# Kernel tuning notes

Measured on AMD Instinct MI355X. Metric: run time of the kernel, lower is better.

## Reference

```python
import jax, jax.numpy as jnp
import numpy as np

N_NODES = 100000
N_EDGES = 1600000
H, D, DE = 4, 32, 32  # heads, node_out_feats, edge_out_feats
NEG_SLOPE = 0.2


def setup_inputs() -> dict:
    key = jax.random.key(0)
    ks = jax.random.split(key, 10)
    return {
        "node_inputs": jax.random.normal(ks[0], (N_NODES, 128), jnp.float32),
        "edge_inputs": jax.random.normal(ks[1], (N_EDGES, 16), jnp.float32),
        "src": jax.random.randint(ks[2], (N_EDGES,), 0, N_NODES, jnp.int32),
        "dst": jax.random.randint(ks[3], (N_EDGES,), 0, N_NODES, jnp.int32),
        "W_fc": jax.random.normal(ks[4], (128, H * D), jnp.float32) * 0.1,
        "attn_src_p": jax.random.normal(ks[5], (1, H, D), jnp.float32) * 0.1,
        "attn_dst_p": jax.random.normal(ks[6], (1, H, D), jnp.float32) * 0.1,
        "W_edge": jax.random.normal(ks[7], (16, H * DE), jnp.float32) * 0.1,
        "attn_edge_p": jax.random.normal(ks[8], (1, H, DE), jnp.float32) * 0.1,
        "W_res": jax.random.normal(ks[9], (128, H * D), jnp.float32) * 0.1,
        "bias_p": jnp.zeros((H * D,), jnp.float32),
    }


def reference(node_inputs, edge_inputs, src, dst, W_fc, attn_src_p,
              attn_dst_p, W_edge, attn_edge_p, W_res, bias_p):
    N = node_inputs.shape[0]
    # node projection: [N, H, D]
    feat = (node_inputs @ W_fc).reshape(N, H, D)
    # per-node attention logits [N, H]
    a_src = (feat * attn_src_p).sum(-1)
    a_dst = (feat * attn_dst_p).sum(-1)
    # edge-feature attention logits [E, H]
    feat_e = (edge_inputs @ W_edge).reshape(-1, H, DE)
    a_edge = (feat_e * attn_edge_p).sum(-1)
    # per-edge score: u_add_v + edge term, then LeakyReLU
    e = a_src[src] + a_dst[dst] + a_edge                 # [E, H]
    e = jnp.where(e > 0, e, NEG_SLOPE * e)
    # edge softmax grouped by destination node
    emax = jax.lax.stop_gradient(jax.ops.segment_max(e, dst, num_segments=N))
    ex = jnp.exp(e - emax[dst])
    denom = jax.ops.segment_sum(ex, dst, num_segments=N)
    attn = ex / denom[dst]                               # [E, H]
    # weighted scatter-aggregate of source features
    msg = feat[src] * attn[:, :, None]                   # [E, H, D]
    x = jax.ops.segment_sum(msg, dst, num_segments=N)    # [N, H, D]
    # residual + bias
    x = x + (node_inputs @ W_res).reshape(N, H, D)
    x = x + bias_p.reshape(H, D)
    return x
```

## Files before the change

### kernel.cpp

```cpp
#include <hip/hip_runtime.h>
#include <math.h>

#define NNODES_FEAT 128
#define HD 128
#define H 4
#define D 32
#define EDGE_F 16
#define NEG_SLOPE 0.2f

typedef _Float16 f16;
typedef _Float16 f16x2 __attribute__((ext_vector_type(2)));
typedef _Float16 f16x4 __attribute__((ext_vector_type(4)));
typedef _Float16 f16x8 __attribute__((ext_vector_type(8)));
typedef float f32x4 __attribute__((ext_vector_type(4)));

union ExPack { float2 f; f16x4 h; };

__global__ void k_wedge(const float* __restrict__ W_edge,
                        const float* __restrict__ attn_edge,
                        float* __restrict__ w_eh) {
    int t = threadIdx.x;
    int k = t >> 2;
    int h = t & 3;
    float s = 0.f;
    for (int d = 0; d < D; ++d)
        s += W_edge[k * HD + h * D + d] * attn_edge[h * D + d];
    w_eh[k * H + h] = s;
}

__global__ __launch_bounds__(256) void k_wt(const float* __restrict__ Wfc,
                                            const float* __restrict__ Wres,
                                            f16* __restrict__ Wt) {
    int i = blockIdx.x * 256 + threadIdx.x;
    int n = i >> 7, k = i & 127;
    float v = (n < 128) ? Wfc[k * HD + n] : Wres[k * HD + (n - 128)];
    Wt[(size_t)n * 128 + k] = (f16)v;
}

#define LDK 136
__global__ __launch_bounds__(256) void k_gemm_mfma(
    const float* __restrict__ A, const f16* __restrict__ Wt,
    const float* __restrict__ bias, f16* __restrict__ feat16,
    float* __restrict__ out, int N) {
    __shared__ f16 As[64 * LDK];
    __shared__ f16 Bs[128 * LDK];
    int tid = threadIdx.x;
    int wave = tid >> 6, lane = tid & 63;
    int m0 = blockIdx.x * 64;

    for (int c = tid; c < 64 * 32; c += 256) {
        int r = c >> 5, cc = (c & 31) * 4;
        int gr = m0 + r;
        float4 v = make_float4(0.f, 0.f, 0.f, 0.f);
        if (gr < N) v = *(const float4*)(A + (size_t)gr * 128 + cc);
        f16x4 h = {(f16)v.x, (f16)v.y, (f16)v.z, (f16)v.w};
        *(f16x4*)(&As[r * LDK + cc]) = h;
    }

    int am = lane & 15, aq = lane >> 4;
    int arow = wave * 16 + am;
    int orow0 = m0 + wave * 16 + aq * 4;

    for (int cb = 0; cb < 2; ++cb) {
        if (cb) __syncthreads();
        const f16* Wblk = Wt + (size_t)cb * 128 * 128;
        for (int c = tid; c < 128 * 16; c += 256) {
            int r = c >> 4, cc = (c & 15) * 8;
            float4 v = *(const float4*)(Wblk + (size_t)r * 128 + cc);
            *(float4*)(&Bs[r * LDK + cc]) = v;
        }
        __syncthreads();

        f32x4 acc[8];
#pragma unroll
        for (int nt = 0; nt < 8; ++nt) acc[nt] = (f32x4){0.f, 0.f, 0.f, 0.f};
#pragma unroll
        for (int kc = 0; kc < 4; ++kc) {
            f16x8 a = *(const f16x8*)(&As[arow * LDK + kc * 32 + aq * 8]);
#pragma unroll
            for (int nt = 0; nt < 8; ++nt) {
                f16x8 b = *(const f16x8*)(&Bs[(nt * 16 + am) * LDK + kc * 32 + aq * 8]);
                acc[nt] = __builtin_amdgcn_mfma_f32_16x16x32_f16(a, b, acc[nt], 0, 0, 0);
            }
        }

        if (cb == 0) {
#pragma unroll
            for (int nt = 0; nt < 8; ++nt) {
                int col = nt * 16 + am;
#pragma unroll
                for (int r = 0; r < 4; ++r) {
                    int row = orow0 + r;
                    if (row < N) feat16[(size_t)row * 128 + col] = (f16)acc[nt][r];
                }
            }
        } else {
#pragma unroll
            for (int nt = 0; nt < 8; ++nt) {
                int col = nt * 16 + am;
                float bv = bias[col];
#pragma unroll
                for (int r = 0; r < 4; ++r) {
                    int row = orow0 + r;
                    if (row < N) out[(size_t)row * 128 + col] = acc[nt][r] + bv;
                }
            }
        }
    }
}

__global__ __launch_bounds__(256) void k_attn_nodes(
    const f16* __restrict__ feat16, const float* __restrict__ attn_src,
    const float* __restrict__ attn_dst, float* __restrict__ a_src,
    float* __restrict__ a_dst, int N) {
    int g = blockIdx.x * 256 + threadIdx.x;
    int n = g >> 2, h = g & 3;
    if (n >= N) return;
    const f16* f = feat16 + (size_t)n * HD + h * D;
    const float* w1 = attn_src + h * D;
    const float* w2 = attn_dst + h * D;
    float s1 = 0.f, s2 = 0.f;
#pragma unroll
    for (int d = 0; d < D; d += 2) {
        f16x2 fv = *(const f16x2*)(f + d);
        float f0 = (float)fv.x, f1 = (float)fv.y;
        s1 += f0 * w1[d] + f1 * w1[d + 1];
        s2 += f0 * w2[d] + f1 * w2[d + 1];
    }
    a_src[n * H + h] = s1;
    a_dst[n * H + h] = s2;
}

__global__ __launch_bounds__(256) void k_count_mlp(
    const float* __restrict__ edge_inputs, const int* __restrict__ dst,
    const float* __restrict__ w_eh, int* __restrict__ deg,
    int* __restrict__ rank, float2* __restrict__ ae16, int E) {
    __shared__ float weh_s[EDGE_F * H];
    if (threadIdx.x < EDGE_F * H) weh_s[threadIdx.x] = w_eh[threadIdx.x];
    __syncthreads();

    int base = blockIdx.x * 512 + threadIdx.x;
    int e0 = base, e1 = base + 256;
    bool v0 = e0 < E, v1 = e1 < E;

    int d0 = v0 ? dst[e0] : 0;
    int d1 = v1 ? dst[e1] : 0;

    float4 xa[4], xb[4];
    if (v0) {
        const float* x = edge_inputs + (size_t)e0 * EDGE_F;
        xa[0] = *(const float4*)(x);      xa[1] = *(const float4*)(x + 4);
        xa[2] = *(const float4*)(x + 8);  xa[3] = *(const float4*)(x + 12);
    }
    if (v1) {
        const float* x = edge_inputs + (size_t)e1 * EDGE_F;
        xb[0] = *(const float4*)(x);      xb[1] = *(const float4*)(x + 4);
        xb[2] = *(const float4*)(x + 8);  xb[3] = *(const float4*)(x + 12);
    }

    int r0 = v0 ? atomicAdd(deg + d0, 1) : 0;
    int r1 = v1 ? atomicAdd(deg + d1, 1) : 0;

    if (v0) {
        float ae0 = 0.f, ae1 = 0.f, ae2 = 0.f, ae3 = 0.f;
        const float* xs = (const float*)xa;
#pragma unroll
        for (int k = 0; k < EDGE_F; ++k) {
            float xv = xs[k];
            ae0 += xv * weh_s[k * H + 0];
            ae1 += xv * weh_s[k * H + 1];
            ae2 += xv * weh_s[k * H + 2];
            ae3 += xv * weh_s[k * H + 3];
        }
        ExPack p;
        p.h = (f16x4){(f16)ae0, (f16)ae1, (f16)ae2, (f16)ae3};
        ae16[e0] = p.f;
        rank[e0] = r0;
    }
    if (v1) {
        float ae0 = 0.f, ae1 = 0.f, ae2 = 0.f, ae3 = 0.f;
        const float* xs = (const float*)xb;
#pragma unroll
        for (int k = 0; k < EDGE_F; ++k) {
            float xv = xs[k];
            ae0 += xv * weh_s[k * H + 0];
            ae1 += xv * weh_s[k * H + 1];
            ae2 += xv * weh_s[k * H + 2];
            ae3 += xv * weh_s[k * H + 3];
        }
        ExPack p;
        p.h = (f16x4){(f16)ae0, (f16)ae1, (f16)ae2, (f16)ae3};
        ae16[e1] = p.f;
        rank[e1] = r1;
    }
}

__global__ __launch_bounds__(256) void k_scan_partial(
    const int* __restrict__ deg, int* __restrict__ partial, int N) {
    __shared__ int sdata[256];
    int t = threadIdx.x;
    int base = blockIdx.x * 1024 + t * 4;
    int s = 0;
#pragma unroll
    for (int j = 0; j < 4; ++j) { int i = base + j; if (i < N) s += deg[i]; }
    sdata[t] = s;
    __syncthreads();
    for (int off = 128; off > 0; off >>= 1) {
        if (t < off) sdata[t] += sdata[t + off];
        __syncthreads();
    }
    if (t == 0) partial[blockIdx.x] = sdata[0];
}

__global__ __launch_bounds__(256) void k_scan_top(
    int* __restrict__ partial, int* __restrict__ offs, int nb, int N) {
    __shared__ int sdata[256];
    int t = threadIdx.x;
    int v = (t < nb) ? partial[t] : 0;
    sdata[t] = v;
    __syncthreads();
    for (int off = 1; off < 256; off <<= 1) {
        int add = (t >= off) ? sdata[t - off] : 0;
        __syncthreads();
        sdata[t] += add;
        __syncthreads();
    }
    int excl = (t == 0) ? 0 : sdata[t - 1];
    if (t < nb) partial[t] = excl;
    if (t == nb - 1) offs[N] = sdata[t];
}

__global__ __launch_bounds__(256) void k_scan_final(
    int* __restrict__ deg_offs, const int* __restrict__ partial, int N) {
    __shared__ int sdata[256];
    int t = threadIdx.x;
    int base = blockIdx.x * 1024 + t * 4;
    int v[4]; int s = 0;
#pragma unroll
    for (int j = 0; j < 4; ++j) { int i = base + j; v[j] = (i < N) ? deg_offs[i] : 0; s += v[j]; }
    sdata[t] = s;
    __syncthreads();
    for (int off = 1; off < 256; off <<= 1) {
        int add = (t >= off) ? sdata[t - off] : 0;
        __syncthreads();
        sdata[t] += add;
        __syncthreads();
    }
    int excl = partial[blockIdx.x] + ((t == 0) ? 0 : sdata[t - 1]);
#pragma unroll
    for (int j = 0; j < 4; ++j) {
        int i = base + j;
        if (i < N) { deg_offs[i] = excl; excl += v[j]; }
    }
}

__global__ __launch_bounds__(256) void k_edge_fill(
    const int* __restrict__ src, const int* __restrict__ dst,
    const int* __restrict__ rank, const float2* __restrict__ ae16,
    const float* __restrict__ a_src, const float* __restrict__ a_dst,
    const int* __restrict__ offs, float4* __restrict__ rec, int E) {
    int base = blockIdx.x * 512 + threadIdx.x;
    int e0 = base, e1 = base + 256;
    bool v0 = e0 < E, v1 = e1 < E;

    int s0 = v0 ? src[e0] : 0, s1 = v1 ? src[e1] : 0;
    int d0 = v0 ? dst[e0] : 0, d1 = v1 ? dst[e1] : 0;
    int r0 = v0 ? rank[e0] : 0, r1 = v1 ? rank[e1] : 0;
    float2 q0 = v0 ? ae16[e0] : make_float2(0.f, 0.f);
    float2 q1 = v1 ? ae16[e1] : make_float2(0.f, 0.f);

    float4 as0 = *(const float4*)(a_src + s0 * H);
    float4 as1 = *(const float4*)(a_src + s1 * H);
    float4 ad0 = *(const float4*)(a_dst + d0 * H);
    float4 ad1 = *(const float4*)(a_dst + d1 * H);
    int p0 = offs[d0] + r0;
    int p1 = offs[d1] + r1;

    if (v0) {
        ExPack qa; qa.f = q0;
        float ev[H];
        ev[0] = as0.x + ad0.x + (float)qa.h[0];
        ev[1] = as0.y + ad0.y + (float)qa.h[1];
        ev[2] = as0.z + ad0.z + (float)qa.h[2];
        ev[3] = as0.w + ad0.w + (float)qa.h[3];
#pragma unroll
        for (int h = 0; h < H; ++h) {
            float t = ev[h];
            t = t > 0.f ? t : NEG_SLOPE * t;
            ev[h] = __expf(t);
        }
        ExPack p;
        p.h = (f16x4){(f16)ev[0], (f16)ev[1], (f16)ev[2], (f16)ev[3]};
        float4 r;
        r.x = __int_as_float(s0);
        r.y = p.f.x;
        r.z = p.f.y;
        r.w = 0.f;
        rec[p0] = r;
    }
    if (v1) {
        ExPack qa; qa.f = q1;
        float ev[H];
        ev[0] = as1.x + ad1.x + (float)qa.h[0];
        ev[1] = as1.y + ad1.y + (float)qa.h[1];
        ev[2] = as1.z + ad1.z + (float)qa.h[2];
        ev[3] = as1.w + ad1.w + (float)qa.h[3];
#pragma unroll
        for (int h = 0; h < H; ++h) {
            float t = ev[h];
            t = t > 0.f ? t : NEG_SLOPE * t;
            ev[h] = __expf(t);
        }
        ExPack p;
        p.h = (f16x4){(f16)ev[0], (f16)ev[1], (f16)ev[2], (f16)ev[3]};
        float4 r;
        r.x = __int_as_float(s1);
        r.y = p.f.x;
        r.z = p.f.y;
        r.w = 0.f;
        rec[p1] = r;
    }
}

__device__ __forceinline__ float exsel(float a, float b, int hword, int hshift) {
    unsigned u = __float_as_uint(hword ? b : a);
    unsigned short us = (unsigned short)(u >> hshift);
    f16 hv;
    __builtin_memcpy(&hv, &us, 2);
    return (float)hv;
}

__global__ __launch_bounds__(256) void k_aggr(
    const f16* __restrict__ feat16, const float4* __restrict__ rec,
    const int* __restrict__ offs, float* __restrict__ out, int N) {
    int wave = threadIdx.x >> 6;
    int lane = threadIdx.x & 63;
    int n = blockIdx.x * 4 + wave;
    if (n >= N) return;
    int beg = offs[n], end = offs[n + 1];
    if (end <= beg) return;
    int hword = (lane >> 5) & 1;
    int hshift = ((lane >> 4) & 1) * 16;
    size_t c0 = (size_t)2 * lane;
    float num0 = 0.f, num1 = 0.f, den = 0.f;
    int i = beg;
    for (; i + 3 < end; i += 4) {
        float4 r0 = rec[i], r1 = rec[i + 1], r2 = rec[i + 2], r3 = rec[i + 3];
        int s0 = __float_as_int(r0.x), s1 = __float_as_int(r1.x);
        int s2 = __float_as_int(r2.x), s3 = __float_as_int(r3.x);
        f16x2 f0 = *(const f16x2*)(feat16 + (size_t)s0 * HD + c0);
        f16x2 f1 = *(const f16x2*)(feat16 + (size_t)s1 * HD + c0);
        f16x2 f2 = *(const f16x2*)(feat16 + (size_t)s2 * HD + c0);
        f16x2 f3 = *(const f16x2*)(feat16 + (size_t)s3 * HD + c0);
        float e0 = exsel(r0.y, r0.z, hword, hshift);
        float e1 = exsel(r1.y, r1.z, hword, hshift);
        float e2 = exsel(r2.y, r2.z, hword, hshift);
        float e3 = exsel(r3.y, r3.z, hword, hshift);
        num0 += e0 * (float)f0.x + e1 * (float)f1.x + e2 * (float)f2.x + e3 * (float)f3.x;
        num1 += e0 * (float)f0.y + e1 * (float)f1.y + e2 * (float)f2.y + e3 * (float)f3.y;
        den += e0 + e1 + e2 + e3;
    }
    for (; i < end; ++i) {
        float4 r0 = rec[i];
        int s0 = __float_as_int(r0.x);
        f16x2 f0 = *(const f16x2*)(feat16 + (size_t)s0 * HD + c0);
        float e0 = exsel(r0.y, r0.z, hword, hshift);
        num0 += e0 * (float)f0.x;
        num1 += e0 * (float)f0.y;
        den += e0;
    }
    float inv = 1.f / den;
    size_t o = (size_t)n * HD + c0;
    float2 v = *(float2*)(out + o);
    v.x += num0 * inv;
    v.y += num1 * inv;
    *(float2*)(out + o) = v;
}

extern "C" void kernel_launch(void* const* d_in, const int* in_sizes, int n_in,
                              void* d_out, int out_size, void* d_ws, size_t ws_size,
                              hipStream_t stream) {
    const float* node_inputs = (const float*)d_in[0];
    const float* edge_inputs = (const float*)d_in[1];
    const int*   src         = (const int*)d_in[2];
    const int*   dst         = (const int*)d_in[3];
    const float* W_fc        = (const float*)d_in[4];
    const float* attn_src_p  = (const float*)d_in[5];
    const float* attn_dst_p  = (const float*)d_in[6];
    const float* W_edge      = (const float*)d_in[7];
    const float* attn_edge_p = (const float*)d_in[8];
    const float* W_res       = (const float*)d_in[9];
    const float* bias_p      = (const float*)d_in[10];

    int N = in_sizes[0] / NNODES_FEAT;
    int E = in_sizes[2];

    float* out = (float*)d_out;

    f16*    feat16  = (f16*)d_ws;
    float4* rec     = (float4*)(feat16 + (size_t)N * HD);
    f16*    Wt      = (f16*)(rec + (size_t)E);
    float*  a_src   = (float*)(Wt + 256 * 128);
    float*  a_dst   = a_src + (size_t)N * H;
    float*  w_eh    = a_dst + (size_t)N * H;
    int*    deg     = (int*)(w_eh + 64);
    int*    offs    = deg;
    int*    partial = deg + (N + 2);
    int*    rank    = partial + 128;
    float2* ae16    = (float2*)(rank + (size_t)E);

    hipMemsetAsync(deg, 0, (size_t)(N + 2) * sizeof(int), stream);

    k_wedge<<<1, 64, 0, stream>>>(W_edge, attn_edge_p, w_eh);
    k_wt<<<(256 * 128) / 256, 256, 0, stream>>>(W_fc, W_res, Wt);

    int gb = (N + 63) / 64;
    k_gemm_mfma<<<gb, 256, 0, stream>>>(node_inputs, Wt, bias_p, feat16, out, N);

    int nb = (N * H + 255) / 256;
    k_attn_nodes<<<nb, 256, 0, stream>>>(feat16, attn_src_p, attn_dst_p, a_src, a_dst, N);

    int eb = (E + 511) / 512;
    k_count_mlp<<<eb, 256, 0, stream>>>(edge_inputs, dst, w_eh, deg, rank, ae16, E);
    int sb = (N + 1023) / 1024;
    k_scan_partial<<<sb, 256, 0, stream>>>(deg, partial, N);
    k_scan_top<<<1, 256, 0, stream>>>(partial, offs, sb, N);
    k_scan_final<<<sb, 256, 0, stream>>>(deg, partial, N);

    k_edge_fill<<<eb, 256, 0, stream>>>(src, dst, rank, ae16, a_src, a_dst,
                                        offs, rec, E);

    int ab = (N + 3) / 4;
    k_aggr<<<ab, 256, 0, stream>>>(feat16, rec, offs, out, N);
}
```

Before: 455.5 us.

## Fuse edge logit and exp into count kernel, split-wave aggregation with wider loads

Moves the per-edge logit, LeakyReLU and exp computation into the degree-counting kernel, so the permute kernel only scatters precomputed values into CSR order with nontemporal stores and 4 edges per thread. The aggregation kernel now splits each wave into two halves that process alternate edges, using 4-wide f16 feature loads and a cross-half shuffle reduction, which halves the serial loop length per node. The attention-node kernel uses 8-wide f16 loads. The trade-off is extra gathers of a_src/a_dst in the atomic-heavy count kernel and more shuffle work per node.

```diff
diff --git a/kernel.cpp b/kernel.cpp
--- a/kernel.cpp
+++ b/kernel.cpp
@@ -121,20 +121,25 @@
     const float* w2 = attn_dst + h * D;
     float s1 = 0.f, s2 = 0.f;
 #pragma unroll
-    for (int d = 0; d < D; d += 2) {
-        f16x2 fv = *(const f16x2*)(f + d);
-        float f0 = (float)fv.x, f1 = (float)fv.y;
-        s1 += f0 * w1[d] + f1 * w1[d + 1];
-        s2 += f0 * w2[d] + f1 * w2[d + 1];
+    for (int dd = 0; dd < D; dd += 8) {
+        f16x8 fv = *(const f16x8*)(f + dd);
+#pragma unroll
+        for (int j = 0; j < 8; ++j) {
+            float fx = (float)fv[j];
+            s1 += fx * w1[dd + j];
+            s2 += fx * w2[dd + j];
+        }
     }
     a_src[n * H + h] = s1;
     a_dst[n * H + h] = s2;
 }
 
-__global__ __launch_bounds__(256) void k_count_mlp(
-    const float* __restrict__ edge_inputs, const int* __restrict__ dst,
-    const float* __restrict__ w_eh, int* __restrict__ deg,
-    int* __restrict__ rank, float2* __restrict__ ae16, int E) {
+__global__ __launch_bounds__(256) void k_edge_logit(
+    const float* __restrict__ edge_inputs, const int* __restrict__ src,
+    const int* __restrict__ dst, const float* __restrict__ w_eh,
+    const float* __restrict__ a_src, const float* __restrict__ a_dst,
+    int* __restrict__ deg, int* __restrict__ rank,
+    float2* __restrict__ evp, int E) {
     __shared__ float weh_s[EDGE_F * H];
     if (threadIdx.x < EDGE_F * H) weh_s[threadIdx.x] = w_eh[threadIdx.x];
     __syncthreads();
@@ -143,8 +148,8 @@
     int e0 = base, e1 = base + 256;
     bool v0 = e0 < E, v1 = e1 < E;
 
-    int d0 = v0 ? dst[e0] : 0;
-    int d1 = v1 ? dst[e1] : 0;
+    int s0 = v0 ? src[e0] : 0, s1 = v1 ? src[e1] : 0;
+    int d0 = v0 ? dst[e0] : 0, d1 = v1 ? dst[e1] : 0;
 
     float4 xa[4], xb[4];
     if (v0) {
@@ -157,6 +162,11 @@
         xb[0] = *(const float4*)(x);      xb[1] = *(const float4*)(x + 4);
         xb[2] = *(const float4*)(x + 8);  xb[3] = *(const float4*)(x + 12);
     }
+
+    float4 as0 = *(const float4*)(a_src + s0 * H);
+    float4 ad0 = *(const float4*)(a_dst + d0 * H);
+    float4 as1 = *(const float4*)(a_src + s1 * H);
+    float4 ad1 = *(const float4*)(a_dst + d1 * H);
 
     int r0 = v0 ? atomicAdd(deg + d0, 1) : 0;
     int r1 = v1 ? atomicAdd(deg + d1, 1) : 0;
@@ -172,9 +182,20 @@
             ae2 += xv * weh_s[k * H + 2];
             ae3 += xv * weh_s[k * H + 3];
         }
+        float ev[H];
+        ev[0] = as0.x + ad0.x + ae0;
+        ev[1] = as0.y + ad0.y + ae1;
+        ev[2] = as0.z + ad0.z + ae2;
+        ev[3] = as0.w + ad0.w + ae3;
+#pragma unroll
+        for (int h = 0; h < H; ++h) {
+            float t = ev[h];
+            t = t > 0.f ? t : NEG_SLOPE * t;
+            ev[h] = __expf(t);
+        }
         ExPack p;
-        p.h = (f16x4){(f16)ae0, (f16)ae1, (f16)ae2, (f16)ae3};
-        ae16[e0] = p.f;
+        p.h = (f16x4){(f16)ev[0], (f16)ev[1], (f16)ev[2], (f16)ev[3]};
+        evp[e0] = p.f;
         rank[e0] = r0;
     }
     if (v1) {
@@ -188,9 +209,20 @@
             ae2 += xv * weh_s[k * H + 2];
             ae3 += xv * weh_s[k * H + 3];
         }
+        float ev[H];
+        ev[0] = as1.x + ad1.x + ae0;
+        ev[1] = as1.y + ad1.y + ae1;
+        ev[2] = as1.z + ad1.z + ae2;
+        ev[3] = as1.w + ad1.w + ae3;
+#pragma unroll
+        for (int h = 0; h < H; ++h) {
+            float t = ev[h];
+            t = t > 0.f ? t : NEG_SLOPE * t;
+            ev[h] = __expf(t);
+        }
         ExPack p;
-        p.h = (f16x4){(f16)ae0, (f16)ae1, (f16)ae2, (f16)ae3};
-        ae16[e1] = p.f;
+        p.h = (f16x4){(f16)ev[0], (f16)ev[1], (f16)ev[2], (f16)ev[3]};
+        evp[e1] = p.f;
         rank[e1] = r1;
     }
 }
@@ -254,71 +286,33 @@
     }
 }
 
-__global__ __launch_bounds__(256) void k_edge_fill(
+__global__ __launch_bounds__(256) void k_permute(
     const int* __restrict__ src, const int* __restrict__ dst,
-    const int* __restrict__ rank, const float2* __restrict__ ae16,
-    const float* __restrict__ a_src, const float* __restrict__ a_dst,
-    const int* __restrict__ offs, float4* __restrict__ rec, int E) {
-    int base = blockIdx.x * 512 + threadIdx.x;
-    int e0 = base, e1 = base + 256;
-    bool v0 = e0 < E, v1 = e1 < E;
-
-    int s0 = v0 ? src[e0] : 0, s1 = v1 ? src[e1] : 0;
-    int d0 = v0 ? dst[e0] : 0, d1 = v1 ? dst[e1] : 0;
-    int r0 = v0 ? rank[e0] : 0, r1 = v1 ? rank[e1] : 0;
-    float2 q0 = v0 ? ae16[e0] : make_float2(0.f, 0.f);
-    float2 q1 = v1 ? ae16[e1] : make_float2(0.f, 0.f);
-
-    float4 as0 = *(const float4*)(a_src + s0 * H);
-    float4 as1 = *(const float4*)(a_src + s1 * H);
-    float4 ad0 = *(const float4*)(a_dst + d0 * H);
-    float4 ad1 = *(const float4*)(a_dst + d1 * H);
-    int p0 = offs[d0] + r0;
-    int p1 = offs[d1] + r1;
-
-    if (v0) {
-        ExPack qa; qa.f = q0;
-        float ev[H];
-        ev[0] = as0.x + ad0.x + (float)qa.h[0];
-        ev[1] = as0.y + ad0.y + (float)qa.h[1];
-        ev[2] = as0.z + ad0.z + (float)qa.h[2];
-        ev[3] = as0.w + ad0.w + (float)qa.h[3];
-#pragma unroll
-        for (int h = 0; h < H; ++h) {
-            float t = ev[h];
-            t = t > 0.f ? t : NEG_SLOPE * t;
-            ev[h] = __expf(t);
-        }
-        ExPack p;
-        p.h = (f16x4){(f16)ev[0], (f16)ev[1], (f16)ev[2], (f16)ev[3]};
-        float4 r;
-        r.x = __int_as_float(s0);
-        r.y = p.f.x;
-        r.z = p.f.y;
-        r.w = 0.f;
-        rec[p0] = r;
-    }
-    if (v1) {
-        ExPack qa; qa.f = q1;
-        float ev[H];
-        ev[0] = as1.x + ad1.x + (float)qa.h[0];
-        ev[1] = as1.y + ad1.y + (float)qa.h[1];
-        ev[2] = as1.z + ad1.z + (float)qa.h[2];
-        ev[3] = as1.w + ad1.w + (float)qa.h[3];
-#pragma unroll
-        for (int h = 0; h < H; ++h) {
-            float t = ev[h];
-            t = t > 0.f ? t : NEG_SLOPE * t;
-            ev[h] = __expf(t);
-        }
-        ExPack p;
-        p.h = (f16x4){(f16)ev[0], (f16)ev[1], (f16)ev[2], (f16)ev[3]};
-        float4 r;
-        r.x = __int_as_float(s1);
-        r.y = p.f.x;
-        r.z = p.f.y;
-        r.w = 0.f;
-        rec[p1] = r;
+    const int* __restrict__ rank, const float2* __restrict__ evp,
+    const int* __restrict__ offs, f32x4* __restrict__ rec, int E) {
+    int base = blockIdx.x * 1024 + threadIdx.x;
+    int s[4], d[4], r[4]; float2 q[4]; bool v[4];
+#pragma unroll
+    for (int j = 0; j < 4; ++j) {
+        int e = base + j * 256;
+        v[j] = e < E;
+        s[j] = v[j] ? src[e] : 0;
+        d[j] = v[j] ? dst[e] : 0;
+        r[j] = v[j] ? rank[e] : 0;
+        q[j] = v[j] ? evp[e] : make_float2(0.f, 0.f);
+    }
+    int pos[4];
+#pragma unroll
+    for (int j = 0; j < 4; ++j) pos[j] = offs[d[j]] + r[j];
+#pragma unroll
+    for (int j = 0; j < 4; ++j) {
+        if (!v[j]) continue;
+        f32x4 rr;
+        rr[0] = __int_as_float(s[j]);
+        rr[1] = q[j].x;
+        rr[2] = q[j].y;
+        rr[3] = 0.f;
+        __builtin_nontemporal_store(rr, &rec[pos[j]]);
     }
 }
 
@@ -331,7 +325,7 @@
 }
 
 __global__ __launch_bounds__(256) void k_aggr(
-    const f16* __restrict__ feat16, const float4* __restrict__ rec,
+    const f16* __restrict__ feat16, const f32x4* __restrict__ rec,
     const int* __restrict__ offs, float* __restrict__ out, int N) {
     int wave = threadIdx.x >> 6;
     int lane = threadIdx.x & 63;
@@ -339,42 +333,64 @@
     if (n >= N) return;
     int beg = offs[n], end = offs[n + 1];
     if (end <= beg) return;
-    int hword = (lane >> 5) & 1;
-    int hshift = ((lane >> 4) & 1) * 16;
-    size_t c0 = (size_t)2 * lane;
-    float num0 = 0.f, num1 = 0.f, den = 0.f;
+    int half = lane >> 5;
+    int l = lane & 31;
+    int hword = (l >> 4) & 1;
+    int hshift = ((l >> 3) & 1) * 16;
+    size_t c0 = (size_t)l * 4;
+    float num0 = 0.f, num1 = 0.f, num2 = 0.f, num3 = 0.f, den = 0.f;
     int i = beg;
     for (; i + 3 < end; i += 4) {
-        float4 r0 = rec[i], r1 = rec[i + 1], r2 = rec[i + 2], r3 = rec[i + 3];
-        int s0 = __float_as_int(r0.x), s1 = __float_as_int(r1.x);
-        int s2 = __float_as_int(r2.x), s3 = __float_as_int(r3.x);
-        f16x2 f0 = *(const f16x2*)(feat16 + (size_t)s0 * HD + c0);
-        f16x2 f1 = *(const f16x2*)(feat16 + (size_t)s1 * HD + c0);
-        f16x2 f2 = *(const f16x2*)(feat16 + (size_t)s2 * HD + c0);
-        f16x2 f3 = *(const f16x2*)(feat16 + (size_t)s3 * HD + c0);
-        float e0 = exsel(r0.y, r0.z, hword, hshift);
-        float e1 = exsel(r1.y, r1.z, hword, hshift);
-        float e2 = exsel(r2.y, r2.z, hword, hshift);
-        float e3 = exsel(r3.y, r3.z, hword, hshift);
-        num0 += e0 * (float)f0.x + e1 * (float)f1.x + e2 * (float)f2.x + e3 * (float)f3.x;
-        num1 += e0 * (float)f0.y + e1 * (float)f1.y + e2 * (float)f2.y + e3 * (float)f3.y;
-        den += e0 + e1 + e2 + e3;
-    }
-    for (; i < end; ++i) {
-        float4 r0 = rec[i];
-        int s0 = __float_as_int(r0.x);
-        f16x2 f0 = *(const f16x2*)(feat16 + (size_t)s0 * HD + c0);
-        float e0 = exsel(r0.y, r0.z, hword, hshift);
-        num0 += e0 * (float)f0.x;
-        num1 += e0 * (float)f0.y;
-        den += e0;
-    }
-    float inv = 1.f / den;
-    size_t o = (size_t)n * HD + c0;
-    float2 v = *(float2*)(out + o);
-    v.x += num0 * inv;
-    v.y += num1 * inv;
-    *(float2*)(out + o) = v;
+        f32x4 ra = __builtin_nontemporal_load(&rec[i + half]);
+        f32x4 rb = __builtin_nontemporal_load(&rec[i + 2 + half]);
+        int sa = __float_as_int(ra[0]), sb = __float_as_int(rb[0]);
+        f16x4 fa = *(const f16x4*)(feat16 + (size_t)sa * HD + c0);
+        f16x4 fb = *(const f16x4*)(feat16 + (size_t)sb * HD + c0);
+        float ea = exsel(ra[1], ra[2], hword, hshift);
+        float eb = exsel(rb[1], rb[2], hword, hshift);
+        num0 += ea * (float)fa[0] + eb * (float)fb[0];
+        num1 += ea * (float)fa[1] + eb * (float)fb[1];
+        num2 += ea * (float)fa[2] + eb * (float)fb[2];
+        num3 += ea * (float)fa[3] + eb * (float)fb[3];
+        den  += ea + eb;
+    }
+    for (; i + 1 < end; i += 2) {
+        f32x4 ra = __builtin_nontemporal_load(&rec[i + half]);
+        int sa = __float_as_int(ra[0]);
+        f16x4 fa = *(const f16x4*)(feat16 + (size_t)sa * HD + c0);
+        float ea = exsel(ra[1], ra[2], hword, hshift);
+        num0 += ea * (float)fa[0];
+        num1 += ea * (float)fa[1];
+        num2 += ea * (float)fa[2];
+        num3 += ea * (float)fa[3];
+        den += ea;
+    }
+    if (i < end) {
+        f32x4 ra = __builtin_nontemporal_load(&rec[i]);
+        int sa = __float_as_int(ra[0]);
+        f16x4 fa = *(const f16x4*)(feat16 + (size_t)sa * HD + c0);
+        float ea = half ? 0.f : exsel(ra[1], ra[2], hword, hshift);
+        num0 += ea * (float)fa[0];
+        num1 += ea * (float)fa[1];
+        num2 += ea * (float)fa[2];
+        num3 += ea * (float)fa[3];
+        den += ea;
+    }
+    num0 += __shfl_xor(num0, 32);
+    num1 += __shfl_xor(num1, 32);
+    num2 += __shfl_xor(num2, 32);
+    num3 += __shfl_xor(num3, 32);
+    den  += __shfl_xor(den, 32);
+    if (half == 0) {
+        float inv = 1.f / den;
+        float* o = out + (size_t)n * HD + c0;
+        float4 v = *(float4*)o;
+        v.x += num0 * inv;
+        v.y += num1 * inv;
+        v.z += num2 * inv;
+        v.w += num3 * inv;
+        *(float4*)o = v;
+    }
 }
 
 extern "C" void kernel_launch(void* const* d_in, const int* in_sizes, int n_in,
@@ -398,7 +414,7 @@
     float* out = (float*)d_out;
 
     f16*    feat16  = (f16*)d_ws;
-    float4* rec     = (float4*)(feat16 + (size_t)N * HD);
+    f32x4*  rec     = (f32x4*)(feat16 + (size_t)N * HD);
     f16*    Wt      = (f16*)(rec + (size_t)E);
     float*  a_src   = (float*)(Wt + 256 * 128);
     float*  a_dst   = a_src + (size_t)N * H;
@@ -407,7 +423,7 @@
     int*    offs    = deg;
     int*    partial = deg + (N + 2);
     int*    rank    = partial + 128;
-    float2* ae16    = (float2*)(rank + (size_t)E);
+    float2* evp     = (float2*)(rank + (size_t)E);
 
     hipMemsetAsync(deg, 0, (size_t)(N + 2) * sizeof(int), stream);
 
@@ -421,14 +437,16 @@
     k_attn_nodes<<<nb, 256, 0, stream>>>(feat16, attn_src_p, attn_dst_p, a_src, a_dst, N);
 
     int eb = (E + 511) / 512;
-    k_count_mlp<<<eb, 256, 0, stream>>>(edge_inputs, dst, w_eh, deg, rank, ae16, E);
+    k_edge_logit<<<eb, 256, 0, stream>>>(edge_inputs, src, dst, w_eh, a_src, a_dst,
+                                         deg, rank, evp, E);
+
     int sb = (N + 1023) / 1024;
     k_scan_partial<<<sb, 256, 0, stream>>>(deg, partial, N);
     k_scan_top<<<1, 256, 0, stream>>>(partial, offs, sb, N);
     k_scan_final<<<sb, 256, 0, stream>>>(deg, partial, N);
 
-    k_edge_fill<<<eb, 256, 0, stream>>>(src, dst, rank, ae16, a_src, a_dst,
-                                        offs, rec, E);
+    int pb = (E + 1023) / 1024;
+    k_permute<<<pb, 256, 0, stream>>>(src, dst, rank, evp, offs, rec, E);
 
     int ab = (N + 3) / 4;
     k_aggr<<<ab, 256, 0, stream>>>(feat16, rec, offs, out, N);
```

Result: slower. 485.7 us (+6.6%).
